# Kernel tuning notes

Hardware: AMD Instinct MI355X
Metric: run time of the kernel (lower is better)

The kernel has to match this reference:

```python
import jax, jax.numpy as jnp
import numpy as np
from jax import lax

B, C, H, W = 2, 96, 96, 96
N = 8            # d_state
R = C // 16      # dt_rank = 6
K = 4            # scan directions


def _gn(x, g, b, eps=1e-5):
    # GroupNorm(num_groups=1): normalize over (C,H,W) per sample, per-channel affine
    mu = jnp.mean(x, axis=(1, 2, 3), keepdims=True)
    var = jnp.var(x, axis=(1, 2, 3), keepdims=True)
    xn = (x - mu) * jax.lax.rsqrt(var + eps)
    return xn * g[None, :, None, None] + b[None, :, None, None]


def _conv1x1(x, w, b):
    return jnp.einsum('bchw,oc->bohw', x, w) + b[None, :, None, None]


def _ss2d(x, xproj_w, dt_w, dt_b, A_log, Ds):
    # x: [B,C,H,W]. 4-directional selective scan (VMamba SS2D core).
    Bn, Cc, Hh, Ww = x.shape
    L = Hh * Ww
    x_hw = x.reshape(Bn, Cc, L)                                   # row-major
    x_wh = jnp.transpose(x, (0, 1, 3, 2)).reshape(Bn, Cc, L)      # col-major
    xs = jnp.stack([x_hw, x_wh, x_hw[..., ::-1], x_wh[..., ::-1]], axis=1)  # [B,K,C,L]
    xdbl = jnp.einsum('bkcl,kdc->bkdl', xs, xproj_w)              # [B,K,R+2N,L]
    dts, Bs, Cs = jnp.split(xdbl, [R, R + N], axis=2)             # [B,K,R,L],[B,K,N,L],[B,K,N,L]
    dts = jax.nn.softplus(jnp.einsum('bkrl,kcr->bkcl', dts, dt_w) + dt_b[None, :, :, None])  # [B,K,C,L]
    A = -jnp.exp(A_log)                                           # [K,C,N]
    dA = jnp.exp(dts[:, :, :, None, :] * A[None, :, :, :, None])                    # [B,K,C,N,L]
    dBx = dts[:, :, :, None, :] * Bs[:, :, None, :, :] * xs[:, :, :, None, :]       # [B,K,C,N,L]

    def comb(e1, e2):
        a1, b1 = e1
        a2, b2 = e2
        return a1 * a2, a2 * b1 + b2

    _, hs = lax.associative_scan(comb, (dA, dBx), axis=-1)        # h_t = dA_t*h_{t-1} + dBx_t
    ys = jnp.einsum('bkcnl,bknl->bkcl', hs, Cs) + Ds[None, :, :, None] * xs
    y0 = ys[:, 0]
    y1 = jnp.transpose(ys[:, 1].reshape(Bn, Cc, Ww, Hh), (0, 1, 3, 2)).reshape(Bn, Cc, L)
    y2 = ys[:, 2][..., ::-1]
    y3 = jnp.transpose(ys[:, 3][..., ::-1].reshape(Bn, Cc, Ww, Hh), (0, 1, 3, 2)).reshape(Bn, Cc, L)
    return (y0 + y1 + y2 + y3).reshape(Bn, Cc, Hh, Ww)


def setup_inputs() -> dict:
    key = jax.random.key(0)
    ks = jax.random.split(key, 12)
    f = lambda k, sh: jax.random.normal(k, sh, jnp.float32) * 0.02
    return {
        'x': jax.random.normal(ks[0], (B, C, H, W), jnp.float32),
        'ln_g': jnp.ones((C,), jnp.float32), 'ln_b': jnp.zeros((C,), jnp.float32),
        'p1_w': f(ks[1], (C, C)), 'p1_b': jnp.zeros((C,), jnp.float32),
        'p2_w': f(ks[2], (C, C)), 'p2_b': jnp.zeros((C,), jnp.float32),
        'dw_w': f(ks[3], (C, 1, 3, 3)), 'dw_b': jnp.zeros((C,), jnp.float32),
        'xproj_w': f(ks[4], (K, R + 2 * N, C)),
        'dt_w': f(ks[5], (K, C, R)), 'dt_b': f(ks[6], (K, C)),
        'A_log': jnp.log(jnp.broadcast_to(jnp.arange(1, N + 1, dtype=jnp.float32), (K, C, N))),
        'Ds': jnp.ones((K, C), jnp.float32),
        'n2_g': jnp.ones((C,), jnp.float32), 'n2_b': jnp.zeros((C,), jnp.float32),
        'ca_w1': f(ks[7], (C // 8, C)), 'ca_b1': jnp.zeros((C // 8,), jnp.float32),
        'ca_w2': f(ks[8], (C, C // 8)), 'ca_b2': jnp.zeros((C,), jnp.float32),
    }


def reference(x, ln_g, ln_b, p1_w, p1_b, p2_w, p2_b, dw_w, dw_b,
              xproj_w, dt_w, dt_b, A_log, Ds, n2_g, n2_b,
              ca_w1, ca_b1, ca_w2, ca_b2):
    h = _gn(x, ln_g, ln_b)
    a = jax.nn.silu(_conv1x1(h, p1_w, p1_b))                       # path 1
    b = _conv1x1(h, p2_w, p2_b)                                    # path 2
    b = lax.conv_general_dilated(b, dw_w, (1, 1), ((1, 1), (1, 1)),
                                 feature_group_count=C,
                                 dimension_numbers=('NCHW', 'OIHW', 'NCHW'))
    b = b + dw_b[None, :, None, None]
    b = jax.nn.silu(b)
    b = _ss2d(b, xproj_w, dt_w, dt_b, A_log, Ds)
    b = _gn(b, n2_g, n2_b)
    y = a * b
    # channel attention (SE-style, reduction 8)
    s = jnp.mean(y, axis=(2, 3))                                   # [B,C]
    z = jax.nn.relu(s @ ca_w1.T + ca_b1)
    attn = jax.nn.sigmoid(z @ ca_w2.T + ca_b2)
    y = y * attn[:, :, None, None]
    return x + y
```

## Files before the change

kernel.cpp:

```cpp
#include <hip/hip_runtime.h>
#include <hip/hip_bf16.h>
#include <cmath>
#include <cstdint>

constexpr int B_ = 2, C_ = 96, H_ = 96, W_ = 96, L_ = H_ * W_;
constexpr int N_ = 8, R_ = 6, K_ = 4, D_ = R_ + 2 * N_;
constexpr int CH_ = 128, G_ = L_ / CH_;
constexpr int JS_ = 4, SEG_ = CH_ / JS_;
constexpr int S_ = G_ * JS_;
constexpr float EPS_ = 1e-5f;

__device__ __forceinline__ float silu_f(float v) { return v / (1.f + __expf(-v)); }
__device__ __forceinline__ float softplus_f(float t) {
    return fmaxf(t, 0.f) + __logf(1.f + __expf(-fabsf(t)));
}

__device__ __forceinline__ void block_reduce2(float& a, float& b) {
    #pragma unroll
    for (int o = 32; o; o >>= 1) { a += __shfl_xor(a, o); b += __shfl_xor(b, o); }
    __shared__ float la[4], lb[4];
    int wid = threadIdx.x >> 6;
    if ((threadIdx.x & 63) == 0) { la[wid] = a; lb[wid] = b; }
    __syncthreads();
    if (threadIdx.x == 0) { a = la[0] + la[1] + la[2] + la[3]; b = lb[0] + lb[1] + lb[2] + lb[3]; }
}

__device__ __forceinline__ void block_reduce4(float& a, float& b, float& c, float& d) {
    #pragma unroll
    for (int o = 32; o; o >>= 1) {
        a += __shfl_xor(a, o); b += __shfl_xor(b, o);
        c += __shfl_xor(c, o); d += __shfl_xor(d, o);
    }
    __shared__ float ls[4][4];
    int wid = threadIdx.x >> 6;
    if ((threadIdx.x & 63) == 0) { ls[wid][0] = a; ls[wid][1] = b; ls[wid][2] = c; ls[wid][3] = d; }
    __syncthreads();
    if (threadIdx.x == 0) {
        a = ls[0][0] + ls[1][0] + ls[2][0] + ls[3][0];
        b = ls[0][1] + ls[1][1] + ls[2][1] + ls[3][1];
        c = ls[0][2] + ls[1][2] + ls[2][2] + ls[3][2];
        d = ls[0][3] + ls[1][3] + ls[2][3] + ls[3][3];
    }
}

__global__ __launch_bounds__(256) void stats_prep_kernel(
    const float* __restrict__ in, float* __restrict__ stats,
    const float* __restrict__ lng, const float* __restrict__ lnb,
    const float* __restrict__ w1, const float* __restrict__ w2,
    float* __restrict__ wmt, float* __restrict__ pq) {
    if (blockIdx.x == 432) {
        if (blockIdx.y != 0) return;
        int t = threadIdx.x;
        if (t >= 192) return;
        int mat = t / 96, o = t % 96;
        const float* w = (mat == 0 ? w1 : w2) + o * C_;
        float* dst = wmt + ((size_t)(mat * 12 + o / 8) * C_) * 8 + (o % 8);
        float P = 0.f, Q = 0.f;
        for (int c = 0; c < C_; ++c) {
            float wv = w[c];
            float g = lng[c];
            P = fmaf(lnb[c], wv, P);
            Q = fmaf(g, wv, Q);
            dst[c * 8] = g * wv;
        }
        pq[mat * 192 + o] = P;
        pq[mat * 192 + 96 + o] = Q;
        return;
    }
    int b = blockIdx.y;
    const float* p = in + (size_t)b * ((size_t)C_ * L_);
    float s = 0.f, s2 = 0.f;
    const int total = C_ * L_;
    for (int i = blockIdx.x * 256 + threadIdx.x; i < total; i += 432 * 256) {
        float v = p[i];
        s += v;
        s2 = fmaf(v, v, s2);
    }
    block_reduce2(s, s2);
    if (threadIdx.x == 0) {
        atomicAdd(&stats[2 * b], s);
        atomicAdd(&stats[2 * b + 1], s2);
    }
}

__global__ __launch_bounds__(256) void conv1x1_kernel(
    const float* __restrict__ x, const float* __restrict__ stats,
    const float* __restrict__ wmt, const float* __restrict__ pq,
    const float* __restrict__ b1, const float* __restrict__ b2,
    float* __restrict__ a, float* __restrict__ bpre) {
    constexpr int OG = 8;
    int b = blockIdx.z, by = blockIdx.y;
    int o0 = by * OG;
    int l = blockIdx.x * 256 + threadIdx.x;

    constexpr float inv = 1.f / (float)(C_ * L_);
    float mu = stats[2 * b] * inv;
    float var = stats[2 * b + 1] * inv - mu * mu;
    float rs = rsqrtf(var + EPS_);

    const float4* w1q = (const float4*)(wmt + ((size_t)(0 * 12 + by) * C_) * 8);
    const float4* w2q = (const float4*)(wmt + ((size_t)(1 * 12 + by) * C_) * 8);

    const float* xb = x + (size_t)b * C_ * L_ + l;
    float acc1[OG], acc2[OG];
    #pragma unroll
    for (int j = 0; j < OG; ++j) { acc1[j] = 0.f; acc2[j] = 0.f; }
    #pragma unroll 4
    for (int c = 0; c < C_; ++c) {
        float xv = xb[(size_t)c * L_];
        float4 wa = w1q[2 * c];
        float4 wb = w1q[2 * c + 1];
        float4 wc = w2q[2 * c];
        float4 wd = w2q[2 * c + 1];
        acc1[0] = fmaf(xv, wa.x, acc1[0]); acc1[1] = fmaf(xv, wa.y, acc1[1]);
        acc1[2] = fmaf(xv, wa.z, acc1[2]); acc1[3] = fmaf(xv, wa.w, acc1[3]);
        acc1[4] = fmaf(xv, wb.x, acc1[4]); acc1[5] = fmaf(xv, wb.y, acc1[5]);
        acc1[6] = fmaf(xv, wb.z, acc1[6]); acc1[7] = fmaf(xv, wb.w, acc1[7]);
        acc2[0] = fmaf(xv, wc.x, acc2[0]); acc2[1] = fmaf(xv, wc.y, acc2[1]);
        acc2[2] = fmaf(xv, wc.z, acc2[2]); acc2[3] = fmaf(xv, wc.w, acc2[3]);
        acc2[4] = fmaf(xv, wd.x, acc2[4]); acc2[5] = fmaf(xv, wd.y, acc2[5]);
        acc2[6] = fmaf(xv, wd.z, acc2[6]); acc2[7] = fmaf(xv, wd.w, acc2[7]);
    }
    float murs = mu * rs;
    #pragma unroll
    for (int j = 0; j < OG; ++j) {
        int o = o0 + j;
        size_t oo = ((size_t)(b * C_ + o)) * L_ + l;
        float be1 = b1[o] + pq[o] - murs * pq[96 + o];
        float be2 = b2[o] + pq[192 + o] - murs * pq[288 + o];
        a[oo] = silu_f(fmaf(rs, acc1[j], be1));
        bpre[oo] = fmaf(rs, acc2[j], be2);
    }
}

__global__ __launch_bounds__(256) void dwt_kernel(const float* __restrict__ bp,
                                                  const float* __restrict__ wgt,
                                                  const float* __restrict__ bias,
                                                  float* __restrict__ u,
                                                  float* __restrict__ u_t) {
    int stripe = blockIdx.x, c = blockIdx.y, b = blockIdx.z;
    int h0 = stripe * 48;
    __shared__ float in_s[50][96];
    __shared__ float out_s[48][97];
    const float* in = bp + ((size_t)(b * C_ + c)) * L_;
    for (int idx = threadIdx.x; idx < 50 * 96; idx += 256) {
        int r = idx / 96, w = idx % 96;
        int hh = h0 - 1 + r;
        in_s[r][w] = (hh >= 0 && hh < 96) ? in[hh * 96 + w] : 0.f;
    }
    __syncthreads();
    const float* kw = wgt + c * 9;
    float k0 = kw[0], k1 = kw[1], k2 = kw[2], k3 = kw[3], k4 = kw[4],
          k5 = kw[5], k6 = kw[6], k7 = kw[7], k8 = kw[8];
    float bs = bias[c];
    float* up = u + ((size_t)(b * C_ + c)) * L_;
    for (int idx = threadIdx.x; idx < 48 * 96; idx += 256) {
        int r = idx / 96, w = idx % 96;
        int ri = r + 1;
        bool wl = (w > 0), wr = (w < 95);
        float acc = bs;
        acc = fmaf(wl ? in_s[ri - 1][w - 1] : 0.f, k0, acc);
        acc = fmaf(in_s[ri - 1][w], k1, acc);
        acc = fmaf(wr ? in_s[ri - 1][w + 1] : 0.f, k2, acc);
        acc = fmaf(wl ? in_s[ri][w - 1] : 0.f, k3, acc);
        acc = fmaf(in_s[ri][w], k4, acc);
        acc = fmaf(wr ? in_s[ri][w + 1] : 0.f, k5, acc);
        acc = fmaf(wl ? in_s[ri + 1][w - 1] : 0.f, k6, acc);
        acc = fmaf(in_s[ri + 1][w], k7, acc);
        acc = fmaf(wr ? in_s[ri + 1][w + 1] : 0.f, k8, acc);
        float v = silu_f(acc);
        up[(h0 + r) * 96 + w] = v;
        out_s[r][w] = v;
    }
    __syncthreads();
    float* tp = u_t + ((size_t)(b * C_ + c)) * L_;
    for (int idx = threadIdx.x; idx < 96 * 48; idx += 256) {
        int w = idx / 48, r = idx % 48;
        tp[w * 96 + h0 + r] = out_s[r][w];
    }
}

__global__ __launch_bounds__(256) void proj_kernel(
    const float* __restrict__ u, const float* __restrict__ u_t,
    const float* __restrict__ xproj,
    float* __restrict__ dts, float* __restrict__ Bsb, float* __restrict__ Csb) {
    int b = blockIdx.z, k = blockIdx.y;
    int pos = threadIdx.x & 63, cg = threadIdx.x >> 6;
    int l = blockIdx.x * 64 + pos;

    __shared__ float sxp[C_][24];
    __shared__ float red[D_][4][64];
    for (int i = threadIdx.x; i < D_ * C_; i += 256) {
        int d = i / C_, c = i % C_;
        sxp[c][d] = xproj[(k * D_ + d) * C_ + c];
    }
    __syncthreads();

    const float* src = ((k & 1) ? u_t : u) + (size_t)b * C_ * L_;
    int posIdx = (k < 2) ? l : (L_ - 1 - l);
    const float* sp = src + (size_t)(cg * 24) * L_ + posIdx;

    float acc[D_];
    #pragma unroll
    for (int d = 0; d < D_; ++d) acc[d] = 0.f;
    #pragma unroll 4
    for (int ci = 0; ci < 24; ++ci) {
        int c = cg * 24 + ci;
        float xv = sp[(size_t)ci * L_];
        float w[22];
        *(float4*)&w[0]  = *(const float4*)&sxp[c][0];
        *(float4*)&w[4]  = *(const float4*)&sxp[c][4];
        *(float4*)&w[8]  = *(const float4*)&sxp[c][8];
        *(float4*)&w[12] = *(const float4*)&sxp[c][12];
        *(float4*)&w[16] = *(const float4*)&sxp[c][16];
        *(float2*)&w[20] = *(const float2*)&sxp[c][20];
        #pragma unroll
        for (int d = 0; d < D_; ++d) acc[d] = fmaf(xv, w[d], acc[d]);
    }
    #pragma unroll
    for (int d = 0; d < D_; ++d) red[d][cg][pos] = acc[d];
    __syncthreads();

    if (cg == 0) {
        #pragma unroll
        for (int r = 0; r < R_; ++r) {
            float s = red[r][0][pos] + red[r][1][pos] + red[r][2][pos] + red[r][3][pos];
            dts[((size_t)((b * K_ + k) * R_ + r)) * L_ + l] = s;
        }
    } else if (cg == 1) {
        #pragma unroll
        for (int n = 0; n < N_; ++n) {
            int d = R_ + n;
            float s = red[d][0][pos] + red[d][1][pos] + red[d][2][pos] + red[d][3][pos];
            Bsb[((size_t)((b * K_ + k) * N_ + n)) * L_ + l] = s;
        }
    } else if (cg == 2) {
        #pragma unroll
        for (int n = 0; n < N_; ++n) {
            int d = R_ + N_ + n;
            float s = red[d][0][pos] + red[d][1][pos] + red[d][2][pos] + red[d][3][pos];
            Csb[((size_t)((b * K_ + k) * N_ + n)) * L_ + l] = s;
        }
    }
}


__global__ __launch_bounds__(192) void scan1_kernel(
    const float* __restrict__ dts, const float* __restrict__ dtw,
    const float* __restrict__ dtbv, const float* __restrict__ Bs,
    const float* __restrict__ u, const float* __restrict__ u_t,
    const float* __restrict__ A_log,
    float* __restrict__ carA, float* __restrict__ carB) {
    int g = blockIdx.x >> 1, chalf = blockIdx.x & 1;
    int k = blockIdx.y, b = blockIdx.z;
    int c0 = chalf * 48;
    const int t = threadIdx.x;
    const int l0 = g * CH_;

    __shared__ float u_s[48][133];
    __shared__ float B_s[128][12];
    __shared__ float T_s[128][8];

    const float* usrc = ((k & 1) ? u_t : u) + (size_t)b * C_ * L_ + (size_t)c0 * L_;
    if (k < 2) {
        for (int idx = t; idx < 48 * 32; idx += 192) {
            int c2 = idx >> 5, q = idx & 31;
            *(float4*)&u_s[c2][q * 4] = *(const float4*)(usrc + (size_t)c2 * L_ + l0 + q * 4);
        }
    } else {
        for (int idx = t; idx < 48 * 32; idx += 192) {
            int c2 = idx >> 5, q = idx & 31;
            float4 v = *(const float4*)(usrc + (size_t)c2 * L_ + (L_ - l0 - q * 4 - 4));
            u_s[c2][q * 4 + 0] = v.w; u_s[c2][q * 4 + 1] = v.z;
            u_s[c2][q * 4 + 2] = v.y; u_s[c2][q * 4 + 3] = v.x;
        }
    }
    const float* Bg = Bs + ((size_t)(b * K_ + k)) * N_ * L_ + l0;
    for (int idx = t; idx < 8 * 32; idx += 192) {
        int n = idx >> 5, q = idx & 31;
        float4 v = *(const float4*)(Bg + (size_t)n * L_ + q * 4);
        B_s[q * 4 + 0][n] = v.x; B_s[q * 4 + 1][n] = v.y;
        B_s[q * 4 + 2][n] = v.z; B_s[q * 4 + 3][n] = v.w;
    }
    const float* Tg = dts + ((size_t)(b * K_ + k)) * R_ * L_ + l0;
    for (int idx = t; idx < 6 * 32; idx += 192) {
        int r = idx >> 5, q = idx & 31;
        float4 v = *(const float4*)(Tg + (size_t)r * L_ + q * 4);
        T_s[q * 4 + 0][r] = v.x; T_s[q * 4 + 1][r] = v.y;
        T_s[q * 4 + 2][r] = v.z; T_s[q * 4 + 3][r] = v.w;
    }
    __syncthreads();

    int cc = t % 48, j = t / 48;
    int c = c0 + cc;
    float A[N_];
    #pragma unroll
    for (int n = 0; n < N_; ++n) A[n] = -__expf(A_log[(k * C_ + c) * N_ + n]);
    float wdt[R_];
    #pragma unroll
    for (int r = 0; r < R_; ++r) wdt[r] = dtw[(k * C_ + c) * R_ + r];
    float bdt = dtbv[k * C_ + c];

    float ap[N_], h[N_];
    #pragma unroll
    for (int n = 0; n < N_; ++n) { ap[n] = 1.f; h[n] = 0.f; }
    int i0 = j * SEG_;
    for (int ii = 0; ii < SEG_; ii += 4) {
        float4 x4 = *(float4*)&u_s[cc][i0 + ii];
        float xx[4] = {x4.x, x4.y, x4.z, x4.w};
        #pragma unroll
        for (int s = 0; s < 4; ++s) {
            int i = i0 + ii + s;
            float4 t4 = *(float4*)&T_s[i][0];
            float2 t2 = *(float2*)&T_s[i][4];
            float tt = bdt;
            tt = fmaf(t4.x, wdt[0], tt); tt = fmaf(t4.y, wdt[1], tt);
            tt = fmaf(t4.z, wdt[2], tt); tt = fmaf(t4.w, wdt[3], tt);
            tt = fmaf(t2.x, wdt[4], tt); tt = fmaf(t2.y, wdt[5], tt);
            float d = softplus_f(tt);
            float dx = d * xx[s];
            float4 ba = *(float4*)&B_s[i][0];
            float4 bb = *(float4*)&B_s[i][4];
            float bv[8] = {ba.x, ba.y, ba.z, ba.w, bb.x, bb.y, bb.z, bb.w};
            #pragma unroll
            for (int n = 0; n < N_; ++n) {
                float da = __expf(d * A[n]);
                ap[n] *= da;
                h[n] = fmaf(da, h[n], bv[n] * dx);
            }
        }
    }
    size_t sidx = (((size_t)((b * K_ + k) * C_ + c)) * S_ + (g * JS_ + j)) * N_;
    #pragma unroll
    for (int n = 0; n < N_; ++n) { carA[sidx + n] = ap[n]; carB[sidx + n] = h[n]; }
}

__global__ __launch_bounds__(256) void scan2_kernel(const float* __restrict__ carA,
                                                    const float* __restrict__ carB,
                                                    float* __restrict__ hinit) {
    int tid = blockIdx.x * 256 + threadIdx.x;
    if (tid >= B_ * K_ * C_ * N_) return;
    int n = tid & 7;
    size_t rowb = (size_t)(tid >> 3) * S_;
    float h = 0.f;
    for (int s = 0; s < S_; s += 8) {
        float av[8], bv[8];
        #pragma unroll
        for (int q = 0; q < 8; ++q) {
            size_t idx = (rowb + s + q) * N_ + n;
            av[q] = carA[idx]; bv[q] = carB[idx];
        }
        #pragma unroll
        for (int q = 0; q < 8; ++q) {
            size_t idx = (rowb + s + q) * N_ + n;
            hinit[idx] = h;
            h = fmaf(av[q], h, bv[q]);
        }
    }
}

__global__ __launch_bounds__(192) void scan3_kernel(
    const float* __restrict__ dts, const float* __restrict__ dtw,
    const float* __restrict__ dtbv, const float* __restrict__ Bs,
    const float* __restrict__ Cs, const float* __restrict__ u,
    const float* __restrict__ u_t, const float* __restrict__ A_log,
    const float* __restrict__ Dsv, const float* __restrict__ hinit,
    float* __restrict__ ydir) {
    int g = blockIdx.x >> 1, chalf = blockIdx.x & 1;
    int k = blockIdx.y, b = blockIdx.z;
    int c0 = chalf * 48;
    const int t = threadIdx.x;
    const int l0 = g * CH_;

    __shared__ float u_s[48][133];
    __shared__ float B_s[128][12];
    __shared__ float C_s[128][12];
    __shared__ float T_s[128][8];

    const float* usrc = ((k & 1) ? u_t : u) + (size_t)b * C_ * L_ + (size_t)c0 * L_;
    if (k < 2) {
        for (int idx = t; idx < 48 * 32; idx += 192) {
            int c2 = idx >> 5, q = idx & 31;
            *(float4*)&u_s[c2][q * 4] = *(const float4*)(usrc + (size_t)c2 * L_ + l0 + q * 4);
        }
    } else {
        for (int idx = t; idx < 48 * 32; idx += 192) {
            int c2 = idx >> 5, q = idx & 31;
            float4 v = *(const float4*)(usrc + (size_t)c2 * L_ + (L_ - l0 - q * 4 - 4));
            u_s[c2][q * 4 + 0] = v.w; u_s[c2][q * 4 + 1] = v.z;
            u_s[c2][q * 4 + 2] = v.y; u_s[c2][q * 4 + 3] = v.x;
        }
    }
    const float* Bg = Bs + ((size_t)(b * K_ + k)) * N_ * L_ + l0;
    const float* Cg = Cs + ((size_t)(b * K_ + k)) * N_ * L_ + l0;
    for (int idx = t; idx < 8 * 32; idx += 192) {
        int n = idx >> 5, q = idx & 31;
        float4 v = *(const float4*)(Bg + (size_t)n * L_ + q * 4);
        B_s[q * 4 + 0][n] = v.x; B_s[q * 4 + 1][n] = v.y;
        B_s[q * 4 + 2][n] = v.z; B_s[q * 4 + 3][n] = v.w;
        float4 w = *(const float4*)(Cg + (size_t)n * L_ + q * 4);
        C_s[q * 4 + 0][n] = w.x; C_s[q * 4 + 1][n] = w.y;
        C_s[q * 4 + 2][n] = w.z; C_s[q * 4 + 3][n] = w.w;
    }
    const float* Tg = dts + ((size_t)(b * K_ + k)) * R_ * L_ + l0;
    for (int idx = t; idx < 6 * 32; idx += 192) {
        int r = idx >> 5, q = idx & 31;
        float4 v = *(const float4*)(Tg + (size_t)r * L_ + q * 4);
        T_s[q * 4 + 0][r] = v.x; T_s[q * 4 + 1][r] = v.y;
        T_s[q * 4 + 2][r] = v.z; T_s[q * 4 + 3][r] = v.w;
    }
    __syncthreads();

    int cc = t % 48, j = t / 48;
    int c = c0 + cc;
    float A[N_];
    #pragma unroll
    for (int n = 0; n < N_; ++n) A[n] = -__expf(A_log[(k * C_ + c) * N_ + n]);
    float wdt[R_];
    #pragma unroll
    for (int r = 0; r < R_; ++r) wdt[r] = dtw[(k * C_ + c) * R_ + r];
    float bdt = dtbv[k * C_ + c];
    float Dv = Dsv[k * C_ + c];

    float h[N_];
    size_t sidx = (((size_t)((b * K_ + k) * C_ + c)) * S_ + (g * JS_ + j)) * N_;
    #pragma unroll
    for (int n = 0; n < N_; ++n) h[n] = hinit[sidx + n];

    int i0 = j * SEG_;
    for (int ii = 0; ii < SEG_; ii += 4) {
        float4 x4 = *(float4*)&u_s[cc][i0 + ii];
        float xx[4] = {x4.x, x4.y, x4.z, x4.w};
        #pragma unroll
        for (int s = 0; s < 4; ++s) {
            int i = i0 + ii + s;
            float4 t4 = *(float4*)&T_s[i][0];
            float2 t2 = *(float2*)&T_s[i][4];
            float tt = bdt;
            tt = fmaf(t4.x, wdt[0], tt); tt = fmaf(t4.y, wdt[1], tt);
            tt = fmaf(t4.z, wdt[2], tt); tt = fmaf(t4.w, wdt[3], tt);
            tt = fmaf(t2.x, wdt[4], tt); tt = fmaf(t2.y, wdt[5], tt);
            float d = softplus_f(tt);
            float dx = d * xx[s];
            float4 ba = *(float4*)&B_s[i][0];
            float4 bb = *(float4*)&B_s[i][4];
            float4 ca = *(float4*)&C_s[i][0];
            float4 cb = *(float4*)&C_s[i][4];
            float bv[8] = {ba.x, ba.y, ba.z, ba.w, bb.x, bb.y, bb.z, bb.w};
            float cv[8] = {ca.x, ca.y, ca.z, ca.w, cb.x, cb.y, cb.z, cb.w};
            float y = Dv * xx[s];
            #pragma unroll
            for (int n = 0; n < N_; ++n) {
                float da = __expf(d * A[n]);
                h[n] = fmaf(da, h[n], bv[n] * dx);
                y = fmaf(cv[n], h[n], y);
            }
            u_s[cc][i] = y;
        }
    }
    __syncthreads();
    float* yg = ydir + ((size_t)((b * K_ + k) * C_ + c0)) * L_ + l0;
    for (int idx = t; idx < 48 * 32; idx += 192) {
        int c2 = idx >> 5, q = idx & 31;
        *(float4*)(yg + (size_t)c2 * L_ + q * 4) = *(float4*)&u_s[c2][q * 4];
    }
}

__global__ __launch_bounds__(256) void merge_kernel(const float* __restrict__ ydir,
                                                    const float* __restrict__ a,
                                                    float* __restrict__ ysum,
                                                    float* __restrict__ stats) {
    int h0 = blockIdx.x * 32;
    int c = blockIdx.y, b = blockIdx.z;
    __shared__ float t1[96][33], t3[96][33];
    const float* y0p = ydir + ((size_t)((b * K_ + 0) * C_ + c)) * L_;
    const float* y1p = ydir + ((size_t)((b * K_ + 1) * C_ + c)) * L_;
    const float* y2p = ydir + ((size_t)((b * K_ + 2) * C_ + c)) * L_;
    const float* y3p = ydir + ((size_t)((b * K_ + 3) * C_ + c)) * L_;
    for (int idx = threadIdx.x; idx < 96 * 32; idx += 256) {
        int w = idx >> 5, hh = idx & 31;
        t1[w][hh] = y1p[w * 96 + h0 + hh];
        t3[w][hh] = y3p[L_ - 1 - (w * 96 + h0 + hh)];
    }
    __syncthreads();
    float s = 0.f, s2 = 0.f, m0 = 0.f, m1 = 0.f;
    float* yout = ysum + ((size_t)(b * C_ + c)) * L_;
    const float* ap = a + ((size_t)(b * C_ + c)) * L_;
    for (int idx = threadIdx.x; idx < 32 * 96; idx += 256) {
        int hh = idx / 96, w = idx % 96;
        int pix = (h0 + hh) * 96 + w;
        float v = y0p[pix] + y2p[L_ - 1 - pix] + t1[w][hh] + t3[w][hh];
        float av = ap[pix];
        yout[pix] = v;
        s += v;
        s2 = fmaf(v, v, s2);
        m0 += av;
        m1 = fmaf(av, v, m1);
    }
    block_reduce4(s, s2, m0, m1);
    if (threadIdx.x == 0) {
        atomicAdd(&stats[4 + 2 * b], s);
        atomicAdd(&stats[5 + 2 * b], s2);
        atomicAdd(&stats[16 + b * C_ + c], m0);
        atomicAdd(&stats[256 + b * C_ + c], m1);
    }
}

__global__ __launch_bounds__(128) void attn_kernel(
    const float* __restrict__ stats, const float* __restrict__ g2,
    const float* __restrict__ b2, const float* __restrict__ w1,
    const float* __restrict__ b1, const float* __restrict__ w2,
    const float* __restrict__ b2a, float* __restrict__ attn) {
    int b = blockIdx.x;
    constexpr float inv = 1.f / (float)(C_ * L_);
    float mu = stats[4 + 2 * b] * inv;
    float var = stats[5 + 2 * b] * inv - mu * mu;
    float rs = rsqrtf(var + EPS_);
    __shared__ float ss[C_];
    __shared__ float zz[12];
    int t = threadIdx.x;
    if (t < C_) {
        float M0 = stats[16 + b * C_ + t];
        float M1 = stats[256 + b * C_ + t];
        ss[t] = (g2[t] * rs * (M1 - mu * M0) + b2[t] * M0) * (1.f / (float)L_);
    }
    __syncthreads();
    if (t < 12) {
        float acc = b1[t];
        for (int c = 0; c < C_; ++c) acc = fmaf(w1[t * C_ + c], ss[c], acc);
        zz[t] = fmaxf(acc, 0.f);
    }
    __syncthreads();
    if (t < C_) {
        float acc = b2a[t];
        #pragma unroll
        for (int j = 0; j < 12; ++j) acc = fmaf(w2[t * 12 + j], zz[j], acc);
        attn[b * C_ + t] = 1.f / (1.f + __expf(-acc));
    }
}

__global__ __launch_bounds__(256) void final_kernel(const float* __restrict__ x,
                                                    const float* __restrict__ ysum,
                                                    const float* __restrict__ a,
                                                    const float* __restrict__ stats,
                                                    const float* __restrict__ g2,
                                                    const float* __restrict__ b2,
                                                    const float* __restrict__ attn,
                                                    float* __restrict__ out) {
    int b = blockIdx.z, c = blockIdx.y;
    int pix = blockIdx.x * 256 + threadIdx.x;
    constexpr float inv = 1.f / (float)(C_ * L_);
    float mu = stats[4 + 2 * b] * inv;
    float var = stats[5 + 2 * b] * inv - mu * mu;
    float rs = rsqrtf(var + EPS_);
    float gc = g2[c] * rs, bc = b2[c] - mu * rs * g2[c];
    float at = attn[b * C_ + c];
    size_t o = ((size_t)(b * C_ + c)) * L_ + pix;
    float bn = fmaf(ysum[o], gc, bc);
    out[o] = fmaf(a[o] * bn, at, x[o]);
}

extern "C" void kernel_launch(void* const* d_in, const int* in_sizes, int n_in,
                              void* d_out, int out_size, void* d_ws, size_t ws_size,
                              hipStream_t stream) {
    const float* x    = (const float*)d_in[0];
    const float* ln_g = (const float*)d_in[1];
    const float* ln_b = (const float*)d_in[2];
    const float* p1w  = (const float*)d_in[3];
    const float* p1b  = (const float*)d_in[4];
    const float* p2w  = (const float*)d_in[5];
    const float* p2b  = (const float*)d_in[6];
    const float* dww  = (const float*)d_in[7];
    const float* dwb  = (const float*)d_in[8];
    const float* xprj = (const float*)d_in[9];
    const float* dtw  = (const float*)d_in[10];
    const float* dtb  = (const float*)d_in[11];
    const float* Alog = (const float*)d_in[12];
    const float* Dsp  = (const float*)d_in[13];
    const float* n2g  = (const float*)d_in[14];
    const float* n2b  = (const float*)d_in[15];
    const float* caw1 = (const float*)d_in[16];
    const float* cab1 = (const float*)d_in[17];
    const float* caw2 = (const float*)d_in[18];
    const float* cab2 = (const float*)d_in[19];
    float* out = (float*)d_out;

    const size_t BCL = (size_t)B_ * C_ * L_ * sizeof(float);
    char* ws = (char*)d_ws;
    size_t off = 0;
    float* stats = (float*)(ws + off); off += 4096;
    float* wmt   = (float*)(ws + off); off += 2 * 12 * 96 * 8 * sizeof(float);
    float* pq    = (float*)(ws + off); off += 2 * 2 * 96 * sizeof(float);
    float* a     = (float*)(ws + off); off += BCL;
    float* bpre  = (float*)(ws + off); off += BCL;
    float* u     = (float*)(ws + off); off += BCL;
    float* u_t   = (float*)(ws + off); off += BCL;
    float* dts   = (float*)(ws + off); off += (size_t)B_ * K_ * R_ * L_ * sizeof(float);
    float* Bsb   = (float*)(ws + off); off += (size_t)B_ * K_ * N_ * L_ * sizeof(float);
    float* Csb   = (float*)(ws + off); off += (size_t)B_ * K_ * N_ * L_ * sizeof(float);
    float* carB  = (float*)(ws + off); off += (size_t)B_ * K_ * C_ * S_ * N_ * sizeof(float);
    float* hinit = (float*)(ws + off); off += (size_t)B_ * K_ * C_ * S_ * N_ * sizeof(float);
    float* ydir  = (float*)(ws + off); off += (size_t)B_ * K_ * C_ * L_ * sizeof(float);
    float* carA = bpre;
    float* ysum = u;
    float* attnv = stats + 512;

    hipMemsetAsync(stats, 0, 4096, stream);

    stats_prep_kernel<<<dim3(433, 2), 256, 0, stream>>>(x, stats, ln_g, ln_b,
                                                        p1w, p2w, wmt, pq);
    conv1x1_kernel<<<dim3(36, 12, 2), 256, 0, stream>>>(x, stats, wmt, pq, p1b, p2b, a, bpre);
    dwt_kernel<<<dim3(2, 96, 2), 256, 0, stream>>>(bpre, dww, dwb, u, u_t);
    proj_kernel<<<dim3(144, 4, 2), 256, 0, stream>>>(u, u_t, xprj, dts, Bsb, Csb);
    scan1_kernel<<<dim3(2 * G_, K_, B_), 192, 0, stream>>>(dts, dtw, dtb, Bsb, u, u_t,
                                                           Alog, carA, carB);
    scan2_kernel<<<24, 256, 0, stream>>>(carA, carB, hinit);
    scan3_kernel<<<dim3(2 * G_, K_, B_), 192, 0, stream>>>(dts, dtw, dtb, Bsb, Csb, u, u_t,
                                                           Alog, Dsp, hinit, ydir);
    merge_kernel<<<dim3(3, 96, 2), 256, 0, stream>>>(ydir, a, ysum, stats);
    attn_kernel<<<2, 128, 0, stream>>>(stats, n2g, n2b, caw1, cab1, caw2, cab2, attnv);
    final_kernel<<<dim3(36, 96, 2), 256, 0, stream>>>(x, ysum, a, stats, n2g, n2b, attnv, out);
}
```

Baseline: 281.1 us.

## Fuse x-projection into scan pass 1 and fold channel attention into final kernel

The x_proj matmul is merged into the first scan kernel. Each block loads all 96 channels of a 128-position chunk once, computes dt/B/C into shared memory and also writes them out for scan3. This avoids a separate launch and a second global read of u. The xproj weights are pre-transposed into a padded layout by an extra block of the stats kernel. The channel-attention MLP is now recomputed redundantly by every block of the final kernel, which removes the attn launch but adds serial work per block. The fused scan kernel uses fewer blocks (G instead of 2G) with more threads and much more shared memory, which may reduce occupancy.

```diff
diff --git a/kernel.cpp b/kernel.cpp
--- a/kernel.cpp
+++ b/kernel.cpp
@@ -47,7 +47,8 @@
     const float* __restrict__ in, float* __restrict__ stats,
     const float* __restrict__ lng, const float* __restrict__ lnb,
     const float* __restrict__ w1, const float* __restrict__ w2,
-    float* __restrict__ wmt, float* __restrict__ pq) {
+    const float* __restrict__ xproj,
+    float* __restrict__ wmt, float* __restrict__ pq, float* __restrict__ xpt) {
     if (blockIdx.x == 432) {
         if (blockIdx.y != 0) return;
         int t = threadIdx.x;
@@ -65,6 +66,18 @@
         }
         pq[mat * 192 + o] = P;
         pq[mat * 192 + 96 + o] = Q;
+        return;
+    }
+    if (blockIdx.x == 433) {
+        if (blockIdx.y != 0) return;
+        for (int e = threadIdx.x; e < K_ * C_ * D_; e += 256) {
+            int k = e / (C_ * D_);
+            int rem = e % (C_ * D_);
+            int c = rem / D_, d = rem % D_;
+            int half = (d >= 11) ? 1 : 0;
+            int jj = d - half * 11;
+            xpt[((size_t)(k * C_ + c)) * 24 + half * 12 + jj] = xproj[(k * D_ + d) * C_ + c];
+        }
         return;
     }
     int b = blockIdx.y;
@@ -180,119 +193,88 @@
     }
 }
 
-__global__ __launch_bounds__(256) void proj_kernel(
+__global__ __launch_bounds__(384) void projscan1_kernel(
     const float* __restrict__ u, const float* __restrict__ u_t,
-    const float* __restrict__ xproj,
-    float* __restrict__ dts, float* __restrict__ Bsb, float* __restrict__ Csb) {
-    int b = blockIdx.z, k = blockIdx.y;
-    int pos = threadIdx.x & 63, cg = threadIdx.x >> 6;
-    int l = blockIdx.x * 64 + pos;
-
-    __shared__ float sxp[C_][24];
-    __shared__ float red[D_][4][64];
-    for (int i = threadIdx.x; i < D_ * C_; i += 256) {
-        int d = i / C_, c = i % C_;
-        sxp[c][d] = xproj[(k * D_ + d) * C_ + c];
-    }
-    __syncthreads();
-
-    const float* src = ((k & 1) ? u_t : u) + (size_t)b * C_ * L_;
-    int posIdx = (k < 2) ? l : (L_ - 1 - l);
-    const float* sp = src + (size_t)(cg * 24) * L_ + posIdx;
-
-    float acc[D_];
-    #pragma unroll
-    for (int d = 0; d < D_; ++d) acc[d] = 0.f;
-    #pragma unroll 4
-    for (int ci = 0; ci < 24; ++ci) {
-        int c = cg * 24 + ci;
-        float xv = sp[(size_t)ci * L_];
-        float w[22];
-        *(float4*)&w[0]  = *(const float4*)&sxp[c][0];
-        *(float4*)&w[4]  = *(const float4*)&sxp[c][4];
-        *(float4*)&w[8]  = *(const float4*)&sxp[c][8];
-        *(float4*)&w[12] = *(const float4*)&sxp[c][12];
-        *(float4*)&w[16] = *(const float4*)&sxp[c][16];
-        *(float2*)&w[20] = *(const float2*)&sxp[c][20];
-        #pragma unroll
-        for (int d = 0; d < D_; ++d) acc[d] = fmaf(xv, w[d], acc[d]);
-    }
-    #pragma unroll
-    for (int d = 0; d < D_; ++d) red[d][cg][pos] = acc[d];
-    __syncthreads();
-
-    if (cg == 0) {
-        #pragma unroll
-        for (int r = 0; r < R_; ++r) {
-            float s = red[r][0][pos] + red[r][1][pos] + red[r][2][pos] + red[r][3][pos];
-            dts[((size_t)((b * K_ + k) * R_ + r)) * L_ + l] = s;
-        }
-    } else if (cg == 1) {
-        #pragma unroll
-        for (int n = 0; n < N_; ++n) {
-            int d = R_ + n;
-            float s = red[d][0][pos] + red[d][1][pos] + red[d][2][pos] + red[d][3][pos];
-            Bsb[((size_t)((b * K_ + k) * N_ + n)) * L_ + l] = s;
-        }
-    } else if (cg == 2) {
-        #pragma unroll
-        for (int n = 0; n < N_; ++n) {
-            int d = R_ + N_ + n;
-            float s = red[d][0][pos] + red[d][1][pos] + red[d][2][pos] + red[d][3][pos];
-            Csb[((size_t)((b * K_ + k) * N_ + n)) * L_ + l] = s;
-        }
-    }
-}
-
-
-__global__ __launch_bounds__(192) void scan1_kernel(
-    const float* __restrict__ dts, const float* __restrict__ dtw,
-    const float* __restrict__ dtbv, const float* __restrict__ Bs,
-    const float* __restrict__ u, const float* __restrict__ u_t,
-    const float* __restrict__ A_log,
+    const float* __restrict__ xpt, const float* __restrict__ dtw,
+    const float* __restrict__ dtbv, const float* __restrict__ A_log,
+    float* __restrict__ dts, float* __restrict__ Bsb, float* __restrict__ Csb,
     float* __restrict__ carA, float* __restrict__ carB) {
-    int g = blockIdx.x >> 1, chalf = blockIdx.x & 1;
-    int k = blockIdx.y, b = blockIdx.z;
-    int c0 = chalf * 48;
+    int g = blockIdx.x, k = blockIdx.y, b = blockIdx.z;
     const int t = threadIdx.x;
     const int l0 = g * CH_;
 
-    __shared__ float u_s[48][133];
+    __shared__ float u_s[96][133];
     __shared__ float B_s[128][12];
     __shared__ float T_s[128][8];
-
-    const float* usrc = ((k & 1) ? u_t : u) + (size_t)b * C_ * L_ + (size_t)c0 * L_;
+    __shared__ float xp_s[96][24];
+
+    const float* usrc = ((k & 1) ? u_t : u) + (size_t)b * C_ * L_;
     if (k < 2) {
-        for (int idx = t; idx < 48 * 32; idx += 192) {
+        for (int idx = t; idx < 96 * 32; idx += 384) {
             int c2 = idx >> 5, q = idx & 31;
             *(float4*)&u_s[c2][q * 4] = *(const float4*)(usrc + (size_t)c2 * L_ + l0 + q * 4);
         }
     } else {
-        for (int idx = t; idx < 48 * 32; idx += 192) {
+        for (int idx = t; idx < 96 * 32; idx += 384) {
             int c2 = idx >> 5, q = idx & 31;
             float4 v = *(const float4*)(usrc + (size_t)c2 * L_ + (L_ - l0 - q * 4 - 4));
             u_s[c2][q * 4 + 0] = v.w; u_s[c2][q * 4 + 1] = v.z;
             u_s[c2][q * 4 + 2] = v.y; u_s[c2][q * 4 + 3] = v.x;
         }
     }
-    const float* Bg = Bs + ((size_t)(b * K_ + k)) * N_ * L_ + l0;
-    for (int idx = t; idx < 8 * 32; idx += 192) {
-        int n = idx >> 5, q = idx & 31;
-        float4 v = *(const float4*)(Bg + (size_t)n * L_ + q * 4);
-        B_s[q * 4 + 0][n] = v.x; B_s[q * 4 + 1][n] = v.y;
-        B_s[q * 4 + 2][n] = v.z; B_s[q * 4 + 3][n] = v.w;
-    }
-    const float* Tg = dts + ((size_t)(b * K_ + k)) * R_ * L_ + l0;
-    for (int idx = t; idx < 6 * 32; idx += 192) {
-        int r = idx >> 5, q = idx & 31;
-        float4 v = *(const float4*)(Tg + (size_t)r * L_ + q * 4);
-        T_s[q * 4 + 0][r] = v.x; T_s[q * 4 + 1][r] = v.y;
-        T_s[q * 4 + 2][r] = v.z; T_s[q * 4 + 3][r] = v.w;
-    }
-    __syncthreads();
-
-    int cc = t % 48, j = t / 48;
-    int c = c0 + cc;
+    const float4* xsrc = (const float4*)(xpt + (size_t)k * C_ * 24);
+    for (int idx = t; idx < 96 * 24 / 4; idx += 384) {
+        ((float4*)xp_s)[idx] = xsrc[idx];
+    }
+    __syncthreads();
+
+    if (t < 256) {
+        int i = t & 127, half = t >> 7;
+        float acc[11];
+        #pragma unroll
+        for (int j = 0; j < 11; ++j) acc[j] = 0.f;
+        const int hb = half * 12;
+        for (int c = 0; c < C_; ++c) {
+            float xv = u_s[c][i];
+            float4 wa = *(const float4*)&xp_s[c][hb];
+            float4 wb = *(const float4*)&xp_s[c][hb + 4];
+            float4 wc = *(const float4*)&xp_s[c][hb + 8];
+            acc[0] = fmaf(xv, wa.x, acc[0]); acc[1] = fmaf(xv, wa.y, acc[1]);
+            acc[2] = fmaf(xv, wa.z, acc[2]); acc[3] = fmaf(xv, wa.w, acc[3]);
+            acc[4] = fmaf(xv, wb.x, acc[4]); acc[5] = fmaf(xv, wb.y, acc[5]);
+            acc[6] = fmaf(xv, wb.z, acc[6]); acc[7] = fmaf(xv, wb.w, acc[7]);
+            acc[8] = fmaf(xv, wc.x, acc[8]); acc[9] = fmaf(xv, wc.y, acc[9]);
+            acc[10] = fmaf(xv, wc.z, acc[10]);
+        }
+        int l = l0 + i;
+        size_t bk = (size_t)(b * K_ + k);
+        if (half == 0) {
+            #pragma unroll
+            for (int r = 0; r < R_; ++r) {
+                dts[(bk * R_ + r) * L_ + l] = acc[r];
+                T_s[i][r] = acc[r];
+            }
+            #pragma unroll
+            for (int n = 0; n < 5; ++n) {
+                Bsb[(bk * N_ + n) * L_ + l] = acc[6 + n];
+                B_s[i][n] = acc[6 + n];
+            }
+        } else {
+            #pragma unroll
+            for (int n = 5; n < 8; ++n) {
+                Bsb[(bk * N_ + n) * L_ + l] = acc[n - 5];
+                B_s[i][n] = acc[n - 5];
+            }
+            #pragma unroll
+            for (int n = 0; n < 8; ++n) {
+                Csb[(bk * N_ + n) * L_ + l] = acc[3 + n];
+            }
+        }
+    }
+    __syncthreads();
+
+    int cc = t % 96, j = t / 96;
+    int c = cc;
     float A[N_];
     #pragma unroll
     for (int n = 0; n < N_; ++n) A[n] = -__expf(A_log[(k * C_ + c) * N_ + n]);
@@ -506,55 +488,43 @@
     }
 }
 
-__global__ __launch_bounds__(128) void attn_kernel(
-    const float* __restrict__ stats, const float* __restrict__ g2,
-    const float* __restrict__ b2, const float* __restrict__ w1,
-    const float* __restrict__ b1, const float* __restrict__ w2,
-    const float* __restrict__ b2a, float* __restrict__ attn) {
-    int b = blockIdx.x;
-    constexpr float inv = 1.f / (float)(C_ * L_);
-    float mu = stats[4 + 2 * b] * inv;
-    float var = stats[5 + 2 * b] * inv - mu * mu;
-    float rs = rsqrtf(var + EPS_);
-    __shared__ float ss[C_];
-    __shared__ float zz[12];
-    int t = threadIdx.x;
-    if (t < C_) {
-        float M0 = stats[16 + b * C_ + t];
-        float M1 = stats[256 + b * C_ + t];
-        ss[t] = (g2[t] * rs * (M1 - mu * M0) + b2[t] * M0) * (1.f / (float)L_);
-    }
-    __syncthreads();
-    if (t < 12) {
-        float acc = b1[t];
-        for (int c = 0; c < C_; ++c) acc = fmaf(w1[t * C_ + c], ss[c], acc);
-        zz[t] = fmaxf(acc, 0.f);
-    }
-    __syncthreads();
-    if (t < C_) {
-        float acc = b2a[t];
-        #pragma unroll
-        for (int j = 0; j < 12; ++j) acc = fmaf(w2[t * 12 + j], zz[j], acc);
-        attn[b * C_ + t] = 1.f / (1.f + __expf(-acc));
-    }
-}
-
-__global__ __launch_bounds__(256) void final_kernel(const float* __restrict__ x,
-                                                    const float* __restrict__ ysum,
-                                                    const float* __restrict__ a,
-                                                    const float* __restrict__ stats,
-                                                    const float* __restrict__ g2,
-                                                    const float* __restrict__ b2,
-                                                    const float* __restrict__ attn,
-                                                    float* __restrict__ out) {
+__global__ __launch_bounds__(256) void final_kernel(
+    const float* __restrict__ x, const float* __restrict__ ysum,
+    const float* __restrict__ a, const float* __restrict__ stats,
+    const float* __restrict__ g2, const float* __restrict__ b2,
+    const float* __restrict__ w1, const float* __restrict__ b1,
+    const float* __restrict__ w2, const float* __restrict__ b2a,
+    float* __restrict__ out) {
     int b = blockIdx.z, c = blockIdx.y;
     int pix = blockIdx.x * 256 + threadIdx.x;
     constexpr float inv = 1.f / (float)(C_ * L_);
     float mu = stats[4 + 2 * b] * inv;
     float var = stats[5 + 2 * b] * inv - mu * mu;
     float rs = rsqrtf(var + EPS_);
+
+    __shared__ float zz[12];
+    __shared__ float atv_s;
+    int t = threadIdx.x;
+    if (t < 12) {
+        float acc = b1[t];
+        for (int cc = 0; cc < C_; ++cc) {
+            float M0 = stats[16 + b * C_ + cc];
+            float M1 = stats[256 + b * C_ + cc];
+            float ss = (g2[cc] * rs * (M1 - mu * M0) + b2[cc] * M0) * (1.f / (float)L_);
+            acc = fmaf(w1[t * C_ + cc], ss, acc);
+        }
+        zz[t] = fmaxf(acc, 0.f);
+    }
+    __syncthreads();
+    if (t == 0) {
+        float acc = b2a[c];
+        #pragma unroll
+        for (int j = 0; j < 12; ++j) acc = fmaf(w2[c * 12 + j], zz[j], acc);
+        atv_s = 1.f / (1.f + __expf(-acc));
+    }
+    __syncthreads();
+    float at = atv_s;
     float gc = g2[c] * rs, bc = b2[c] - mu * rs * g2[c];
-    float at = attn[b * C_ + c];
     size_t o = ((size_t)(b * C_ + c)) * L_ + pix;
     float bn = fmaf(ysum[o], gc, bc);
     out[o] = fmaf(a[o] * bn, at, x[o]);
@@ -591,6 +561,7 @@
     float* stats = (float*)(ws + off); off += 4096;
     float* wmt   = (float*)(ws + off); off += 2 * 12 * 96 * 8 * sizeof(float);
     float* pq    = (float*)(ws + off); off += 2 * 2 * 96 * sizeof(float);
+    float* xpt   = (float*)(ws + off); off += (size_t)K_ * C_ * 24 * sizeof(float);
     float* a     = (float*)(ws + off); off += BCL;
     float* bpre  = (float*)(ws + off); off += BCL;
     float* u     = (float*)(ws + off); off += BCL;
@@ -603,21 +574,19 @@
     float* ydir  = (float*)(ws + off); off += (size_t)B_ * K_ * C_ * L_ * sizeof(float);
     float* carA = bpre;
     float* ysum = u;
-    float* attnv = stats + 512;
 
     hipMemsetAsync(stats, 0, 4096, stream);
 
-    stats_prep_kernel<<<dim3(433, 2), 256, 0, stream>>>(x, stats, ln_g, ln_b,
-                                                        p1w, p2w, wmt, pq);
+    stats_prep_kernel<<<dim3(434, 2), 256, 0, stream>>>(x, stats, ln_g, ln_b,
+                                                        p1w, p2w, xprj, wmt, pq, xpt);
     conv1x1_kernel<<<dim3(36, 12, 2), 256, 0, stream>>>(x, stats, wmt, pq, p1b, p2b, a, bpre);
     dwt_kernel<<<dim3(2, 96, 2), 256, 0, stream>>>(bpre, dww, dwb, u, u_t);
-    proj_kernel<<<dim3(144, 4, 2), 256, 0, stream>>>(u, u_t, xprj, dts, Bsb, Csb);
-    scan1_kernel<<<dim3(2 * G_, K_, B_), 192, 0, stream>>>(dts, dtw, dtb, Bsb, u, u_t,
-                                                           Alog, carA, carB);
+    projscan1_kernel<<<dim3(G_, K_, B_), 384, 0, stream>>>(u, u_t, xpt, dtw, dtb, Alog,
+                                                           dts, Bsb, Csb, carA, carB);
     scan2_kernel<<<24, 256, 0, stream>>>(carA, carB, hinit);
     scan3_kernel<<<dim3(2 * G_, K_, B_), 192, 0, stream>>>(dts, dtw, dtb, Bsb, Csb, u, u_t,
                                                            Alog, Dsp, hinit, ydir);
     merge_kernel<<<dim3(3, 96, 2), 256, 0, stream>>>(ydir, a, ysum, stats);
-    attn_kernel<<<2, 128, 0, stream>>>(stats, n2g, n2b, caw1, cab1, caw2, cab2, attnv);
-    final_kernel<<<dim3(36, 96, 2), 256, 0, stream>>>(x, ysum, a, stats, n2g, n2b, attnv, out);
-}
+    final_kernel<<<dim3(36, 96, 2), 256, 0, stream>>>(x, ysum, a, stats, n2g, n2b,
+                                                      caw1, cab1, caw2, cab2, out);
+}
```

New measurement: 295.6 us. 5.2% more time.

## Parallelize carry-propagation scan with per-row blocks and warp-level prefix scan

Applied to the files above, without the earlier changes.

The middle stage of the chunked selective scan previously ran one serial thread per (b,k,c,n) row across all 288 segments, using only 24 blocks. It now launches one block per (b,k,c), loads the segment carries into shared memory with vectorized loads, and has 32 lanes per state run a local 9-segment reduction followed by a shuffle-based associative prefix scan. The intent is to remove the long serial dependency chain and the low occupancy of this stage. In exchange it adds shared-memory traffic, shuffles and a change in floating-point summation order.

```diff
diff --git a/kernel.cpp b/kernel.cpp
--- a/kernel.cpp
+++ b/kernel.cpp
@@ -243,7 +243,6 @@
         }
     }
 }
-
 
 __global__ __launch_bounds__(192) void scan1_kernel(
     const float* __restrict__ dts, const float* __restrict__ dtw,
@@ -338,25 +337,45 @@
 __global__ __launch_bounds__(256) void scan2_kernel(const float* __restrict__ carA,
                                                     const float* __restrict__ carB,
                                                     float* __restrict__ hinit) {
-    int tid = blockIdx.x * 256 + threadIdx.x;
-    if (tid >= B_ * K_ * C_ * N_) return;
-    int n = tid & 7;
-    size_t rowb = (size_t)(tid >> 3) * S_;
-    float h = 0.f;
-    for (int s = 0; s < S_; s += 8) {
-        float av[8], bv[8];
-        #pragma unroll
-        for (int q = 0; q < 8; ++q) {
-            size_t idx = (rowb + s + q) * N_ + n;
-            av[q] = carA[idx]; bv[q] = carB[idx];
-        }
-        #pragma unroll
-        for (int q = 0; q < 8; ++q) {
-            size_t idx = (rowb + s + q) * N_ + n;
-            hinit[idx] = h;
-            h = fmaf(av[q], h, bv[q]);
-        }
-    }
+    int row = blockIdx.x;
+    const int t = threadIdx.x;
+    __shared__ float as_[S_ * N_];
+    __shared__ float bs_[S_ * N_];
+    const float4* Ag = (const float4*)(carA + (size_t)row * S_ * N_);
+    const float4* Bg4 = (const float4*)(carB + (size_t)row * S_ * N_);
+    float4* As4 = (float4*)as_;
+    float4* Bs4 = (float4*)bs_;
+    for (int i = t; i < S_ * N_ / 4; i += 256) { As4[i] = Ag[i]; Bs4[i] = Bg4[i]; }
+    __syncthreads();
+
+    int n = t >> 5, g = t & 31;
+    int s0 = g * 9;
+    float A = 1.f, Bc = 0.f;
+    #pragma unroll
+    for (int q = 0; q < 9; ++q) {
+        int idx = (s0 + q) * N_ + n;
+        float a = as_[idx], b = bs_[idx];
+        Bc = fmaf(a, Bc, b);
+        A = a * A;
+    }
+    #pragma unroll
+    for (int d = 1; d < 32; d <<= 1) {
+        float pA = __shfl_up(A, d, 32);
+        float pB = __shfl_up(Bc, d, 32);
+        if (g >= d) { Bc = fmaf(A, pB, Bc); A = A * pA; }
+    }
+    float h = __shfl_up(Bc, 1, 32);
+    if (g == 0) h = 0.f;
+    #pragma unroll
+    for (int q = 0; q < 9; ++q) {
+        int idx = (s0 + q) * N_ + n;
+        float a = as_[idx], b = bs_[idx];
+        as_[idx] = h;
+        h = fmaf(a, h, b);
+    }
+    __syncthreads();
+    float4* Hg = (float4*)(hinit + (size_t)row * S_ * N_);
+    for (int i = t; i < S_ * N_ / 4; i += 256) Hg[i] = As4[i];
 }
 
 __global__ __launch_bounds__(192) void scan3_kernel(
@@ -614,7 +633,7 @@
     proj_kernel<<<dim3(144, 4, 2), 256, 0, stream>>>(u, u_t, xprj, dts, Bsb, Csb);
     scan1_kernel<<<dim3(2 * G_, K_, B_), 192, 0, stream>>>(dts, dtw, dtb, Bsb, u, u_t,
                                                            Alog, carA, carB);
-    scan2_kernel<<<24, 256, 0, stream>>>(carA, carB, hinit);
+    scan2_kernel<<<B_ * K_ * C_, 256, 0, stream>>>(carA, carB, hinit);
     scan3_kernel<<<dim3(2 * G_, K_, B_), 192, 0, stream>>>(dts, dtw, dtb, Bsb, Csb, u, u_t,
                                                            Alog, Dsp, hinit, ydir);
     merge_kernel<<<dim3(3, 96, 2), 256, 0, stream>>>(ydir, a, ysum, stats);
```

Measured after the change: 269.9 us. 4.0% less time.
